# Optimization experiments

Hardware: AMD Instinct MI355X
Metric: run time of the kernel (lower is better)

Reference implementation:

```python
import jax, jax.numpy as jnp
import numpy as np

N = 50000      # num nodes
E = 800000     # num edges
IN_DIM = 128
OUT_DIM = 128
HEADS = 4
HEAD_DIM = OUT_DIM // HEADS  # concat=True
TAU = 1.0


def setup_inputs() -> dict:
    key = jax.random.key(0)
    ks = jax.random.split(key, 8)
    x = jax.random.normal(ks[0], (N, IN_DIM), dtype=jnp.float32)
    edge_index = jax.random.randint(ks[1], (2, E), 0, N, dtype=jnp.int64)
    # xavier-uniform-ish linear weights, stored as (in, out) so y = x @ W
    def xavier(k, fan_in, fan_out):
        limit = np.sqrt(6.0 / (fan_in + fan_out)).astype(np.float32)
        return jax.random.uniform(k, (fan_in, fan_out), jnp.float32, -limit, limit)
    Wt = xavier(ks[2], IN_DIM, HEADS * HEAD_DIM)
    Ws = xavier(ks[3], IN_DIM, HEADS * HEAD_DIM)
    Wc = xavier(ks[4], IN_DIM, HEADS * HEAD_DIM)
    Wout = xavier(ks[5], HEADS * HEAD_DIM, OUT_DIM)
    bout = jnp.zeros((OUT_DIM,), jnp.float32)
    return {"x": x, "edge_index": edge_index, "Wt": Wt, "Ws": Ws,
            "Wc": Wc, "Wout": Wout, "bout": bout}


def reference(x, edge_index, Wt, Ws, Wc, Wout, bout):
    src = edge_index[0]  # j (source of message)
    dst = edge_index[1]  # i (target, softmax group)
    q = (x @ Wt).reshape(N, HEADS, HEAD_DIM)
    k = (x @ Ws).reshape(N, HEADS, HEAD_DIM)
    v = (x @ Wc).reshape(N, HEADS, HEAD_DIM)
    # per-edge dot-product scores: (E, H)
    scores = jnp.einsum('ehd,ehd->eh', q[dst], k[src]) / TAU
    # segment softmax over incoming edges of each dst node
    m = jax.ops.segment_max(scores, dst, num_segments=N)        # (N, H)
    e = jnp.exp(scores - m[dst])                                # (E, H)
    denom = jax.ops.segment_sum(e, dst, num_segments=N)         # (N, H)
    alpha = e / denom[dst]                                      # (E, H)
    # weighted scatter-add aggregation
    msg = v[src] * alpha[:, :, None]                            # (E, H, D)
    agg = jax.ops.segment_sum(msg, dst, num_segments=N)         # (N, H, D)
    out = agg.reshape(N, HEADS * HEAD_DIM) @ Wout + bout
    out = jax.nn.relu(out)
    # residual: in_dim == out_dim -> identity projection
    return out + x
```

## Files before the change

kernel.cpp:

```cpp
#include <hip/hip_runtime.h>
#include <hip/hip_bf16.h>

#define HEADS 4
#define HEAD_DIM 32
#define SLAB 128

typedef __bf16 bf16x8 __attribute__((ext_vector_type(8)));
typedef float  f32x4  __attribute__((ext_vector_type(4)));
typedef _Float16 h2   __attribute__((ext_vector_type(2)));

__device__ __forceinline__ unsigned short f2bf(float f) {
    unsigned u = __float_as_uint(f);
    u += 0x7fffu + ((u >> 16) & 1u);
    return (unsigned short)(u >> 16);
}
__device__ __forceinline__ unsigned pack2bf(float a, float b) {
    return (unsigned)f2bf(a) | ((unsigned)f2bf(b) << 16);
}
__device__ __forceinline__ float2 bf2f(unsigned u) {
    return make_float2(__uint_as_float(u << 16),
                       __uint_as_float(u & 0xffff0000u));
}
__device__ __forceinline__ unsigned short f2h(float f) {
    _Float16 h = (_Float16)f;
    return *(unsigned short*)&h;
}

__global__ __launch_bounds__(256) void fillw_kernel(
    const float* __restrict__ W0, const float* __restrict__ W1,
    const float* __restrict__ W2, const float* __restrict__ W3,
    unsigned short* __restrict__ Wsw,
    const int* __restrict__ edge, int E,
    int* __restrict__ cnt, int* __restrict__ col)
{
    if (blockIdx.x < 32) {
        const float* Wm[4] = { W0, W1, W2, W3 };
        int mi = blockIdx.x >> 3;
        const float* __restrict__ W = Wm[mi];
        unsigned short* __restrict__ o = Wsw + (size_t)mi * 16384;
        int t = (blockIdx.x & 7) * 256 + threadIdx.x;
        int kg = t >> 7;
        int n  = t & 127;
        ushort4 p0, p1;
        p0.x = f2bf(W[(kg * 8 + 0) * 128 + n]);
        p0.y = f2bf(W[(kg * 8 + 1) * 128 + n]);
        p0.z = f2bf(W[(kg * 8 + 2) * 128 + n]);
        p0.w = f2bf(W[(kg * 8 + 3) * 128 + n]);
        p1.x = f2bf(W[(kg * 8 + 4) * 128 + n]);
        p1.y = f2bf(W[(kg * 8 + 5) * 128 + n]);
        p1.z = f2bf(W[(kg * 8 + 6) * 128 + n]);
        p1.w = f2bf(W[(kg * 8 + 7) * 128 + n]);
        *(ushort4*)(o + kg * 1024 + n * 8)     = p0;
        *(ushort4*)(o + kg * 1024 + n * 8 + 4) = p1;
    } else {
        int e = (blockIdx.x - 32) * 256 + threadIdx.x;
        if (e < E) {
            int dst = edge[E + e];
            int src = edge[e];
            int pos = atomicAdd(&cnt[dst], 1);
            if (pos < SLAB)
                col[(size_t)dst * SLAB + pos] = src;
        }
    }
}

__device__ __forceinline__ void mfma_compute64g(
    const unsigned short* As, const unsigned short* __restrict__ Bsw,
    f32x4 (&acc)[2][4], int mb, int nb, int quad, int l16)
{
    #pragma unroll
    for (int a = 0; a < 2; a++)
        #pragma unroll
        for (int b = 0; b < 4; b++)
            #pragma unroll
            for (int e = 0; e < 4; e++) acc[a][b][e] = 0.f;

    #pragma unroll
    for (int kk = 0; kk < 4; kk++) {
        bf16x8 af[2], bf[4];
        #pragma unroll
        for (int mt = 0; mt < 2; mt++)
            af[mt] = *(const bf16x8*)(As + (mb + mt * 16 + l16) * 136
                                         + kk * 32 + quad * 8);
        #pragma unroll
        for (int nt = 0; nt < 4; nt++)
            bf[nt] = *(const bf16x8*)(Bsw + (kk * 4 + quad) * 1024
                                          + (nb + nt * 16 + l16) * 8);
        #pragma unroll
        for (int mt = 0; mt < 2; mt++)
            #pragma unroll
            for (int nt = 0; nt < 4; nt++)
                acc[mt][nt] = __builtin_amdgcn_mfma_f32_16x16x32_bf16(
                    af[mt], bf[nt], acc[mt][nt], 0, 0, 0);
    }
}

__global__ __launch_bounds__(256) void qkv_kernel(
    const float* __restrict__ x, const unsigned short* __restrict__ Wsw,
    unsigned short* __restrict__ qh, unsigned short* __restrict__ kh,
    unsigned short* __restrict__ vh, int M)
{
    __shared__ __align__(16) unsigned short As[64 * 136];
    const int r0 = blockIdx.x * 64;
    const int t  = threadIdx.x;

    #pragma unroll
    for (int it = 0; it < 4; it++) {
        int c   = t + it * 256;
        int row = c >> 4, kp = c & 15;
        float4 a = make_float4(0.f, 0.f, 0.f, 0.f);
        float4 b = make_float4(0.f, 0.f, 0.f, 0.f);
        if (r0 + row < M) {
            a = *(const float4*)(x + (size_t)(r0 + row) * 128 + kp * 8);
            b = *(const float4*)(x + (size_t)(r0 + row) * 128 + kp * 8 + 4);
        }
        uint4 pk;
        pk.x = pack2bf(a.x, a.y);
        pk.y = pack2bf(a.z, a.w);
        pk.z = pack2bf(b.x, b.y);
        pk.w = pack2bf(b.z, b.w);
        *(uint4*)(As + row * 136 + kp * 8) = pk;
    }
    __syncthreads();

    const int wave = t >> 6, L = t & 63;
    const int quad = L >> 4, l16 = L & 15;
    const int mb = (wave >> 1) * 32;
    const int nb = (wave & 1) * 64;

    #pragma unroll
    for (int mode = 0; mode < 3; mode++) {
        f32x4 acc[2][4];
        mfma_compute64g(As, Wsw + (size_t)mode * 16384, acc, mb, nb, quad, l16);

        unsigned short* ob = (mode == 0) ? qh : (mode == 1) ? kh : vh;
        #pragma unroll
        for (int mt = 0; mt < 2; mt++) {
            #pragma unroll
            for (int nt = 0; nt < 4; nt++) {
                int colj = nb + nt * 16 + l16;
                #pragma unroll
                for (int r = 0; r < 4; r++) {
                    int row = r0 + mb + mt * 16 + quad * 4 + r;
                    if (row < M) {
                        float val = acc[mt][nt][r];
                        ob[(size_t)row * 128 + colj] =
                            (mode == 2) ? f2bf(val) : f2h(val);
                    }
                }
            }
        }
    }
}

__global__ __launch_bounds__(256) void out_mfma_kernel(
    const unsigned short* __restrict__ aggh, const unsigned short* __restrict__ Wsw,
    const float* __restrict__ bout, const float* __restrict__ x,
    float* __restrict__ out, int M)
{
    __shared__ __align__(16) unsigned short As[64 * 136];
    const int r0 = blockIdx.x * 64;
    const int t  = threadIdx.x;

    #pragma unroll
    for (int it = 0; it < 4; it++) {
        int c   = t + it * 256;
        int row = c >> 4, kp = c & 15;
        uint4 val = make_uint4(0, 0, 0, 0);
        if (r0 + row < M)
            val = *(const uint4*)(aggh + (size_t)(r0 + row) * 128 + kp * 8);
        *(uint4*)(As + row * 136 + kp * 8) = val;
    }
    __syncthreads();

    const int wave = t >> 6, L = t & 63;
    const int quad = L >> 4, l16 = L & 15;
    const int mb = (wave >> 1) * 32;
    const int nb = (wave & 1) * 64;

    f32x4 acc[2][4];
    mfma_compute64g(As, Wsw, acc, mb, nb, quad, l16);

    #pragma unroll
    for (int mt = 0; mt < 2; mt++) {
        #pragma unroll
        for (int nt = 0; nt < 4; nt++) {
            int colj = nb + nt * 16 + l16;
            float b = bout[colj];
            #pragma unroll
            for (int r = 0; r < 4; r++) {
                int row = r0 + mb + mt * 16 + quad * 4 + r;
                if (row < M) {
                    float val = fmaxf(acc[mt][nt][r] + b, 0.f)
                              + x[(size_t)row * 128 + colj];
                    out[(size_t)row * 128 + colj] = val;
                }
            }
        }
    }
}

__global__ __launch_bounds__(256) void attn_kernel(
    const unsigned short* __restrict__ qhB, const unsigned short* __restrict__ kh,
    const unsigned short* __restrict__ vh,
    const int* __restrict__ cnt, const int* __restrict__ col,
    unsigned short* __restrict__ aggh, int N)
{
    const int wv   = threadIdx.x >> 6;
    const int lane = threadIdx.x & 63;
    const int dst  = blockIdx.x * 4 + wv;
    if (dst >= N) return;

    __shared__ __align__(16) unsigned short kbuf[4][16 * 136];
    __shared__ __align__(16) float swW[4][64];

    const int deg = min(cnt[dst], SLAB);
    const size_t orow = (size_t)dst * 128;
    const size_t slab = (size_t)dst * SLAB;

    if (deg == 0) {
        *(unsigned*)(aggh + orow + 2 * lane) = 0u;
        return;
    }

    const int h    = lane & 3;
    const int eo   = lane >> 2;
    const int hv   = lane >> 4;
    const int rr   = lane >> 4;
    const int cseg = (lane & 15) * 8;

    uint4 qreg[4];
    {
        const uint4* qp = (const uint4*)(qhB + orow + h * HEAD_DIM);
        qreg[0] = qp[0]; qreg[1] = qp[1]; qreg[2] = qp[2]; qreg[3] = qp[3];
    }
    const h2* qh = (const h2*)qreg;

    int srcA = 0, srcB = 0;
    if (lane < deg) srcA = col[slab + lane];
    if (64 + lane < deg) srcB = col[slab + 64 + lane];

    float sreg[8];
    #pragma unroll
    for (int c = 0; c < 8; c++) {
        sreg[c] = -3.4e38f;
        if (c * 16 < deg) {
            const int nle  = deg - c * 16;
            const int csrc = (c < 4) ? srcA : srcB;
            const int lsel = (c & 3) * 16;
            #pragma unroll
            for (int i = 0; i < 4; i++) {
                int r  = i * 4 + rr;
                int sr = __shfl(csrc, lsel + r);
                uint4 kv = *(const uint4*)(kh + (size_t)sr * 128 + cseg);
                *(uint4*)(&kbuf[wv][r * 136 + cseg]) = kv;
            }
            if (eo < nle) {
                const unsigned short* kb = &kbuf[wv][eo * 136 + h * 32];
                uint4 u0 = *(const uint4*)(kb);
                uint4 u1 = *(const uint4*)(kb + 8);
                uint4 u2 = *(const uint4*)(kb + 16);
                uint4 u3 = *(const uint4*)(kb + 24);
                const h2* p0 = (const h2*)&u0;
                const h2* p1 = (const h2*)&u1;
                const h2* p2 = (const h2*)&u2;
                const h2* p3 = (const h2*)&u3;
                float a = 0.f;
                #pragma unroll
                for (int j = 0; j < 4; j++) {
#if __has_builtin(__builtin_amdgcn_fdot2)
                    a = __builtin_amdgcn_fdot2(qh[j],      p0[j], a, false);
                    a = __builtin_amdgcn_fdot2(qh[4 + j],  p1[j], a, false);
                    a = __builtin_amdgcn_fdot2(qh[8 + j],  p2[j], a, false);
                    a = __builtin_amdgcn_fdot2(qh[12 + j], p3[j], a, false);
#else
                    h2 w0 = qh[j] * p0[j], w1 = qh[4+j] * p1[j];
                    h2 w2 = qh[8+j] * p2[j], w3 = qh[12+j] * p3[j];
                    a += (float)w0[0] + (float)w0[1] + (float)w1[0] + (float)w1[1]
                       + (float)w2[0] + (float)w2[1] + (float)w3[0] + (float)w3[1];
#endif
                }
                sreg[c] = a;
            }
        }
    }

    float m = sreg[0];
    #pragma unroll
    for (int c = 1; c < 8; c++) m = fmaxf(m, sreg[c]);
    #pragma unroll
    for (int off = 4; off < 64; off <<= 1)
        m = fmaxf(m, __shfl_xor(m, off));

    float dsum = 0.f, acc0 = 0.f, acc1 = 0.f;
    #pragma unroll
    for (int c = 0; c < 8; c++) {
        if (c * 16 < deg) {
            const int nle  = min(16, deg - c * 16);
            const int csrc = (c < 4) ? srcA : srcB;
            const int lsel = (c & 3) * 16;
            float ev = (eo < nle) ? __expf(sreg[c] - m) : 0.f;
            dsum += ev;
            swW[wv][lane] = ev;
            if (nle == 16) {
                #pragma unroll
                for (int j = 0; j < 16; j++) {
                    int   sj = __shfl(csrc, lsel + j);
                    float w  = swW[wv][j * 4 + hv];
                    unsigned uv = *(const unsigned*)(vh + (size_t)sj * 128 + 2 * lane);
                    float2 vvv = bf2f(uv);
                    acc0 = fmaf(w, vvv.x, acc0);
                    acc1 = fmaf(w, vvv.y, acc1);
                }
            } else {
                for (int j = 0; j < nle; j++) {
                    int   sj = __shfl(csrc, lsel + j);
                    float w  = swW[wv][j * 4 + hv];
                    unsigned uv = *(const unsigned*)(vh + (size_t)sj * 128 + 2 * lane);
                    float2 vvv = bf2f(uv);
                    acc0 = fmaf(w, vvv.x, acc0);
                    acc1 = fmaf(w, vvv.y, acc1);
                }
            }
        }
    }

    #pragma unroll
    for (int off = 4; off < 64; off <<= 1)
        dsum += __shfl_xor(dsum, off);
    float d = __shfl(dsum, hv);
    unsigned short lo = f2bf(acc0 / d);
    unsigned short hi = f2bf(acc1 / d);
    *(unsigned*)(aggh + orow + 2 * lane) = (unsigned)lo | ((unsigned)hi << 16);
}

extern "C" void kernel_launch(void* const* d_in, const int* in_sizes, int n_in,
                              void* d_out, int out_size, void* d_ws, size_t ws_size,
                              hipStream_t stream)
{
    const float* x    = (const float*)d_in[0];
    const int*   edge = (const int*)d_in[1];
    const float* Wt   = (const float*)d_in[2];
    const float* Ws   = (const float*)d_in[3];
    const float* Wc   = (const float*)d_in[4];
    const float* Wout = (const float*)d_in[5];
    const float* bout = (const float*)d_in[6];
    float* out = (float*)d_out;

    const int N = in_sizes[0] / 128;
    const int E = in_sizes[1] / 2;

    unsigned short* qh   = (unsigned short*)d_ws;
    unsigned short* kh   = qh   + (size_t)N * 128;
    unsigned short* vh   = kh   + (size_t)N * 128;
    unsigned short* aggh = vh   + (size_t)N * 128;
    unsigned short* Wsw  = aggh + (size_t)N * 128;
    int* cnt  = (int*)(Wsw + 4 * 16384);
    int* colb = cnt + ((N + 3) & ~3);

    hipMemsetAsync(cnt, 0, (size_t)N * sizeof(int), stream);

    const int gE   = (E + 255) / 256;
    const int gM64 = (N + 63) / 64;

    fillw_kernel<<<32 + gE, 256, 0, stream>>>(Wt, Ws, Wc, Wout, Wsw,
                                              edge, E, cnt, colb);
    qkv_kernel<<<gM64, 256, 0, stream>>>(x, Wsw, qh, kh, vh, N);
    attn_kernel<<<(N + 3) / 4, 256, 0, stream>>>(qh, kh, vh, cnt, colb, aggh, N);
    out_mfma_kernel<<<gM64, 256, 0, stream>>>(aggh, Wsw + 3 * 16384, bout, x, out, N);
}
```

Before: 232.0 us.

## Rewrite attention kernel with online softmax and register-direct key loads

Replaces the two-pass attention (scores buffered in registers, then exp and aggregate) with a single-pass online softmax that keeps a running max and rescales the accumulators per 16-edge chunk. Keys are now read straight into registers per lane instead of being staged through LDS, and the value gather is split across two half-waves that each load 4 fp16 values per lane. V is now stored as fp16 instead of bf16. The kernel also adds an occupancy hint on launch bounds. This removes shared memory and the bf16 conversion, at the cost of extra shuffles and reductions per chunk and a cross-half reduction at the end.

```diff
diff --git a/kernel.cpp b/kernel.cpp
--- a/kernel.cpp
+++ b/kernel.cpp
@@ -16,10 +16,6 @@
 }
 __device__ __forceinline__ unsigned pack2bf(float a, float b) {
     return (unsigned)f2bf(a) | ((unsigned)f2bf(b) << 16);
-}
-__device__ __forceinline__ float2 bf2f(unsigned u) {
-    return make_float2(__uint_as_float(u << 16),
-                       __uint_as_float(u & 0xffff0000u));
 }
 __device__ __forceinline__ unsigned short f2h(float f) {
     _Float16 h = (_Float16)f;
@@ -142,11 +138,8 @@
                 #pragma unroll
                 for (int r = 0; r < 4; r++) {
                     int row = r0 + mb + mt * 16 + quad * 4 + r;
-                    if (row < M) {
-                        float val = acc[mt][nt][r];
-                        ob[(size_t)row * 128 + colj] =
-                            (mode == 2) ? f2bf(val) : f2h(val);
-                    }
+                    if (row < M)
+                        ob[(size_t)row * 128 + colj] = f2h(acc[mt][nt][r]);
                 }
             }
         }
@@ -200,7 +193,7 @@
     }
 }
 
-__global__ __launch_bounds__(256) void attn_kernel(
+__global__ __launch_bounds__(256, 8) void attn_kernel(
     const unsigned short* __restrict__ qhB, const unsigned short* __restrict__ kh,
     const unsigned short* __restrict__ vh,
     const int* __restrict__ cnt, const int* __restrict__ col,
@@ -211,127 +204,121 @@
     const int dst  = blockIdx.x * 4 + wv;
     if (dst >= N) return;
 
-    __shared__ __align__(16) unsigned short kbuf[4][16 * 136];
-    __shared__ __align__(16) float swW[4][64];
-
-    const int deg = min(cnt[dst], SLAB);
     const size_t orow = (size_t)dst * 128;
     const size_t slab = (size_t)dst * SLAB;
 
-    if (deg == 0) {
-        *(unsigned*)(aggh + orow + 2 * lane) = 0u;
-        return;
-    }
-
     const int h    = lane & 3;
     const int eo   = lane >> 2;
-    const int hv   = lane >> 4;
-    const int rr   = lane >> 4;
-    const int cseg = (lane & 15) * 8;
-
+    const int half = lane >> 5;
+    const int li   = lane & 31;
+    const int hvv  = li >> 3;
+
+    const int degr = cnt[dst];
+    const int colv = col[slab + lane];
     uint4 qreg[4];
     {
         const uint4* qp = (const uint4*)(qhB + orow + h * HEAD_DIM);
         qreg[0] = qp[0]; qreg[1] = qp[1]; qreg[2] = qp[2]; qreg[3] = qp[3];
     }
-    const h2* qh = (const h2*)qreg;
-
-    int srcA = 0, srcB = 0;
-    if (lane < deg) srcA = col[slab + lane];
+    const h2* qv = (const h2*)qreg;
+
+    const int deg = min(degr, SLAB);
+    if (deg == 0) {
+        *(unsigned*)(aggh + orow + 2 * lane) = 0u;
+        return;
+    }
+    const int srcA = (lane < deg) ? colv : 0;
+    int srcB = 0;
     if (64 + lane < deg) srcB = col[slab + 64 + lane];
 
-    float sreg[8];
-    #pragma unroll
-    for (int c = 0; c < 8; c++) {
-        sreg[c] = -3.4e38f;
-        if (c * 16 < deg) {
-            const int nle  = deg - c * 16;
-            const int csrc = (c < 4) ? srcA : srcB;
-            const int lsel = (c & 3) * 16;
-            #pragma unroll
-            for (int i = 0; i < 4; i++) {
-                int r  = i * 4 + rr;
-                int sr = __shfl(csrc, lsel + r);
-                uint4 kv = *(const uint4*)(kh + (size_t)sr * 128 + cseg);
-                *(uint4*)(&kbuf[wv][r * 136 + cseg]) = kv;
-            }
-            if (eo < nle) {
-                const unsigned short* kb = &kbuf[wv][eo * 136 + h * 32];
-                uint4 u0 = *(const uint4*)(kb);
-                uint4 u1 = *(const uint4*)(kb + 8);
-                uint4 u2 = *(const uint4*)(kb + 16);
-                uint4 u3 = *(const uint4*)(kb + 24);
-                const h2* p0 = (const h2*)&u0;
-                const h2* p1 = (const h2*)&u1;
-                const h2* p2 = (const h2*)&u2;
-                const h2* p3 = (const h2*)&u3;
-                float a = 0.f;
-                #pragma unroll
-                for (int j = 0; j < 4; j++) {
+    float m_p  = -1e30f;
+    float dsum = 0.f;
+    float a0 = 0.f, a1 = 0.f, a2 = 0.f, a3 = 0.f;
+
+    const int nchunk = (deg + 15) >> 4;
+    for (int c = 0; c < nchunk; ++c) {
+        const int nle  = min(16, deg - c * 16);
+        const int csrc = (c < 4) ? srcA : srcB;
+        const int lsel = (c & 3) * 16;
+
+        const int sr = __shfl(csrc, lsel + eo);
+        uint4 kreg[4];
+        {
+            const uint4* kp = (const uint4*)(kh + (size_t)sr * 128 + h * HEAD_DIM);
+            kreg[0] = kp[0]; kreg[1] = kp[1]; kreg[2] = kp[2]; kreg[3] = kp[3];
+        }
+        const h2* kv = (const h2*)kreg;
+        float s0 = 0.f, s1 = 0.f, s2 = 0.f, s3 = 0.f;
+        #pragma unroll
+        for (int j = 0; j < 4; ++j) {
 #if __has_builtin(__builtin_amdgcn_fdot2)
-                    a = __builtin_amdgcn_fdot2(qh[j],      p0[j], a, false);
-                    a = __builtin_amdgcn_fdot2(qh[4 + j],  p1[j], a, false);
-                    a = __builtin_amdgcn_fdot2(qh[8 + j],  p2[j], a, false);
-                    a = __builtin_amdgcn_fdot2(qh[12 + j], p3[j], a, false);
+            s0 = __builtin_amdgcn_fdot2(qv[j],      kv[j],      s0, false);
+            s1 = __builtin_amdgcn_fdot2(qv[4 + j],  kv[4 + j],  s1, false);
+            s2 = __builtin_amdgcn_fdot2(qv[8 + j],  kv[8 + j],  s2, false);
+            s3 = __builtin_amdgcn_fdot2(qv[12 + j], kv[12 + j], s3, false);
 #else
-                    h2 w0 = qh[j] * p0[j], w1 = qh[4+j] * p1[j];
-                    h2 w2 = qh[8+j] * p2[j], w3 = qh[12+j] * p3[j];
-                    a += (float)w0[0] + (float)w0[1] + (float)w1[0] + (float)w1[1]
-                       + (float)w2[0] + (float)w2[1] + (float)w3[0] + (float)w3[1];
+            h2 w0 = qv[j] * kv[j],         w1 = qv[4 + j] * kv[4 + j];
+            h2 w2 = qv[8 + j] * kv[8 + j], w3 = qv[12 + j] * kv[12 + j];
+            s0 += (float)w0[0] + (float)w0[1];
+            s1 += (float)w1[0] + (float)w1[1];
+            s2 += (float)w2[0] + (float)w2[1];
+            s3 += (float)w3[0] + (float)w3[1];
 #endif
-                }
-                sreg[c] = a;
-            }
-        }
-    }
-
-    float m = sreg[0];
-    #pragma unroll
-    for (int c = 1; c < 8; c++) m = fmaxf(m, sreg[c]);
-    #pragma unroll
-    for (int off = 4; off < 64; off <<= 1)
-        m = fmaxf(m, __shfl_xor(m, off));
-
-    float dsum = 0.f, acc0 = 0.f, acc1 = 0.f;
-    #pragma unroll
-    for (int c = 0; c < 8; c++) {
-        if (c * 16 < deg) {
-            const int nle  = min(16, deg - c * 16);
-            const int csrc = (c < 4) ? srcA : srcB;
-            const int lsel = (c & 3) * 16;
-            float ev = (eo < nle) ? __expf(sreg[c] - m) : 0.f;
-            dsum += ev;
-            swW[wv][lane] = ev;
-            if (nle == 16) {
-                #pragma unroll
-                for (int j = 0; j < 16; j++) {
-                    int   sj = __shfl(csrc, lsel + j);
-                    float w  = swW[wv][j * 4 + hv];
-                    unsigned uv = *(const unsigned*)(vh + (size_t)sj * 128 + 2 * lane);
-                    float2 vvv = bf2f(uv);
-                    acc0 = fmaf(w, vvv.x, acc0);
-                    acc1 = fmaf(w, vvv.y, acc1);
-                }
-            } else {
-                for (int j = 0; j < nle; j++) {
-                    int   sj = __shfl(csrc, lsel + j);
-                    float w  = swW[wv][j * 4 + hv];
-                    unsigned uv = *(const unsigned*)(vh + (size_t)sj * 128 + 2 * lane);
-                    float2 vvv = bf2f(uv);
-                    acc0 = fmaf(w, vvv.x, acc0);
-                    acc1 = fmaf(w, vvv.y, acc1);
-                }
-            }
-        }
-    }
-
-    #pragma unroll
-    for (int off = 4; off < 64; off <<= 1)
-        dsum += __shfl_xor(dsum, off);
-    float d = __shfl(dsum, hv);
-    unsigned short lo = f2bf(acc0 / d);
-    unsigned short hi = f2bf(acc1 / d);
-    *(unsigned*)(aggh + orow + 2 * lane) = (unsigned)lo | ((unsigned)hi << 16);
+        }
+        float s = (s0 + s1) + (s2 + s3);
+        s = (eo < nle) ? s : -1e30f;
+
+        float cm = s;
+        #pragma unroll
+        for (int off = 4; off < 64; off <<= 1)
+            cm = fmaxf(cm, __shfl_xor(cm, off));
+
+        const float mp_new   = fmaxf(m_p, cm);
+        const float scale_p  = __expf(m_p - mp_new);
+        const float ev = (eo < nle) ? __expf(s - mp_new) : 0.f;
+        m_p = mp_new;
+
+        float cs = ev;
+        #pragma unroll
+        for (int off = 4; off < 64; off <<= 1)
+            cs += __shfl_xor(cs, off);
+
+        const float scale = __shfl(scale_p, hvv);
+        const float cs_v  = __shfl(cs, hvv);
+        dsum = dsum * scale + cs_v;
+        a0 *= scale; a1 *= scale; a2 *= scale; a3 *= scale;
+
+        const int nj = (nle + 1) >> 1;
+        for (int jj = 0; jj < nj; ++jj) {
+            const int   j  = 2 * jj + half;
+            const int   sj = __shfl(csrc, lsel + j);
+            const float w  = __shfl(ev, j * 4 + hvv);
+            const uint2 uv = *(const uint2*)(vh + (size_t)sj * 128 + 4 * li);
+            const h2 va = __builtin_bit_cast(h2, uv.x);
+            const h2 vb = __builtin_bit_cast(h2, uv.y);
+            a0 = fmaf(w, (float)va[0], a0);
+            a1 = fmaf(w, (float)va[1], a1);
+            a2 = fmaf(w, (float)vb[0], a2);
+            a3 = fmaf(w, (float)vb[1], a3);
+        }
+    }
+
+    a0 += __shfl_xor(a0, 32);
+    a1 += __shfl_xor(a1, 32);
+    a2 += __shfl_xor(a2, 32);
+    a3 += __shfl_xor(a3, 32);
+
+    const float inv = __builtin_amdgcn_rcpf(dsum);
+    a0 *= inv; a1 *= inv; a2 *= inv; a3 *= inv;
+
+    const int sl = lane >> 1;
+    const float b0 = __shfl(a0, sl);
+    const float b1 = __shfl(a1, sl);
+    const float b2 = __shfl(a2, sl);
+    const float b3 = __shfl(a3, sl);
+    const float o0 = (lane & 1) ? b2 : b0;
+    const float o1 = (lane & 1) ? b3 : b1;
+    *(unsigned*)(aggh + orow + 2 * lane) = pack2bf(o0, o1);
 }
 
 extern "C" void kernel_launch(void* const* d_in, const int* in_sizes, int n_in,
```

Result: no change. 232.0 us (+0.0%).
